# Optimization experiments

Hardware: AMD Instinct MI355X
Metric: run time of the kernel (lower is better)

## Reference

```python
import jax, jax.numpy as jnp
import numpy as np

K = 16
TAU = 0.2
BN_EPS = 1e-5


def setup_inputs() -> dict:
    key = jax.random.key(0)
    ks = jax.random.split(key, 8)
    B, C, N = 2, 128, 8192
    c_hidden, c_out, se_hidden = 128, 128, 8
    x = jax.random.normal(ks[0], (B, C, N), dtype=jnp.float32)
    pos = jax.random.normal(ks[1], (B, 3, N), dtype=jnp.float32)
    # conv1x1 weights (kaiming-ish scale), BN gamma/beta, SE linears (xavier-ish)
    w1 = jax.random.normal(ks[2], (c_hidden, 2 * C), dtype=jnp.float32) * jnp.sqrt(2.0 / c_hidden)
    w2 = jax.random.normal(ks[3], (c_out, c_hidden), dtype=jnp.float32) * jnp.sqrt(2.0 / c_out)
    g1 = jnp.ones((c_hidden,), jnp.float32); b1 = jnp.zeros((c_hidden,), jnp.float32)
    g2 = jnp.ones((c_out,), jnp.float32); b2 = jnp.zeros((c_out,), jnp.float32)
    fc1_w = jax.random.normal(ks[4], (se_hidden, c_out), dtype=jnp.float32) * jnp.sqrt(2.0 / (se_hidden + c_out))
    fc1_b = jnp.zeros((se_hidden,), jnp.float32)
    fc2_w = jax.random.normal(ks[5], (c_out, se_hidden), dtype=jnp.float32) * jnp.sqrt(2.0 / (se_hidden + c_out))
    fc2_b = jnp.zeros((c_out,), jnp.float32)
    return {"x": x, "pos": pos, "w1": w1, "g1": g1, "b1": b1, "w2": w2, "g2": g2, "b2": b2,
            "fc1_w": fc1_w, "fc1_b": fc1_b, "fc2_w": fc2_w, "fc2_b": fc2_b}


def _batchnorm(h, gamma, beta):
    # h: [B, N, C]; training-mode BN over (B, N) with biased variance
    mean = jnp.mean(h, axis=(0, 1), keepdims=True)
    var = jnp.mean((h - mean) ** 2, axis=(0, 1), keepdims=True)
    return (h - mean) * jax.lax.rsqrt(var + BN_EPS) * gamma + beta


def _forward(x, pos, w1, g1, b1, w2, g2, b2, fc1_w, fc1_b, fc2_w, fc2_b):
    x = jnp.nan_to_num(x, nan=0.0, posinf=1e4, neginf=-1e4)
    pos = jnp.nan_to_num(pos, nan=0.0, posinf=1e4, neginf=-1e4)
    B, C, N = x.shape
    x_t = jnp.transpose(x, (0, 2, 1))        # [B, N, C]
    p_t = jnp.transpose(pos, (0, 2, 1))      # [B, N, 3]

    # KNN via full pairwise squared distances (same ordering as torch.cdist topk smallest)
    sq = jnp.sum(p_t * p_t, axis=-1)         # [B, N]
    d2 = sq[:, :, None] + sq[:, None, :] - 2.0 * jnp.einsum('bnd,bmd->bnm', p_t, p_t)  # [B, N, N]
    _, idx = jax.lax.top_k(-d2, K)           # [B, N, K] indices of K nearest (incl. self)
    idx = jax.lax.stop_gradient(idx)

    bidx = jnp.arange(B)[:, None, None]
    neigh_x = x_t[bidx, idx]                 # [B, N, K, C]
    neigh_p = p_t[bidx, idx]                 # [B, N, K, 3]

    diff = neigh_p - p_t[:, :, None, :]
    d = jnp.sqrt(jnp.sum(diff * diff, axis=-1))          # [B, N, K]
    d = jnp.maximum(d, 1e-6)
    w = jax.nn.softmax(-d / TAU, axis=-1)                # [B, N, K]
    agg = jnp.einsum('bnkc,bnk->bnc', neigh_x, w)        # [B, N, C]

    fuse = jnp.concatenate([x_t, agg], axis=-1)          # [B, N, 2C]
    h = jax.nn.relu(_batchnorm(jnp.einsum('bnc,hc->bnh', fuse, w1), g1, b1))
    y = jax.nn.relu(_batchnorm(jnp.einsum('bnh,oh->bno', h, w2), g2, b2))  # [B, N, C_out]

    # SE: global average pool over N, two-layer gate
    s = jnp.mean(y, axis=1)                               # [B, C_out]
    gate = jax.nn.sigmoid(jax.nn.relu(s @ fc1_w.T + fc1_b) @ fc2_w.T + fc2_b)
    y = y * gate[:, None, :]

    y = x_t + y                                           # residual (c_in == c_out)
    return jnp.transpose(y, (0, 2, 1))                    # [B, C_out, N]


def reference(x, pos, w1, g1, b1, w2, g2, b2, fc1_w, fc1_b, fc2_w, fc2_b):
    return _forward(x, pos, w1, g1, b1, w2, g2, b2, fc1_w, fc1_b, fc2_w, fc2_b)
```

## Files before the change

### kernel.cpp

```cpp
#include <hip/hip_runtime.h>
#include <math.h>

#define NPTS 8192
#define NB 2
#define CCH 128
#define KNN 16

typedef __attribute__((ext_vector_type(2))) float f32x2;

__global__ __launch_bounds__(256) void k_zero(float* __restrict__ p) {
  p[blockIdx.x * 256 + threadIdx.x] = 0.f;
}

__device__ __forceinline__ int spread4(int v) {
  return (v & 1) | ((v & 2) << 2) | ((v & 4) << 4) | ((v & 8) << 6);
}
__device__ __forceinline__ int cell_of(float x, float y, float z) {
  int cx = (int)fminf(fmaxf((x + 4.f) * 2.f, 0.f), 15.f);
  int cy = (int)fminf(fmaxf((y + 4.f) * 2.f, 0.f), 15.f);
  int cz = (int)fminf(fmaxf((z + 4.f) * 2.f, 0.f), 15.f);
  return spread4(cx) | (spread4(cy) << 1) | (spread4(cz) << 2);
}

__global__ __launch_bounds__(256) void k_hist(const float* __restrict__ pos,
                                              int* __restrict__ hist) {
  int i = blockIdx.x * 256 + threadIdx.x;
  int b = i >> 13, n = i & 8191;
  const float* p = pos + (size_t)b * 3 * NPTS;
  int c = cell_of(p[n], p[NPTS + n], p[2 * NPTS + n]);
  atomicAdd(&hist[b * 4096 + c], 1);
}

__global__ __launch_bounds__(1024) void k_scan(const int* __restrict__ hist,
                                               int* __restrict__ hoff) {
  __shared__ int part[1024];
  int t = threadIdx.x;
  int v[8];
  int s = 0;
#pragma unroll
  for (int i = 0; i < 8; ++i) { v[i] = hist[t * 8 + i]; s += v[i]; }
  part[t] = s;
  __syncthreads();
  for (int off = 1; off < 512; off <<= 1) {
    int add = ((t & 511) >= off) ? part[t - off] : 0;
    __syncthreads();
    part[t] += add;
    __syncthreads();
  }
  int ex = part[t] - s;
#pragma unroll
  for (int i = 0; i < 8; ++i) { hoff[t * 8 + i] = ex; ex += v[i]; }
}

__global__ __launch_bounds__(256) void k_scatter(const float* __restrict__ pos,
                                                 int* __restrict__ hoff,
                                                 float4* __restrict__ spos,
                                                 int* __restrict__ rank) {
  int i = blockIdx.x * 256 + threadIdx.x;
  int b = i >> 13, n = i & 8191;
  const float* p = pos + (size_t)b * 3 * NPTS;
  float x = p[n], y = p[NPTS + n], z = p[2 * NPTS + n];
  int c = cell_of(x, y, z);
  int slot = atomicAdd(&hoff[b * 4096 + c], 1);
  spos[(b << 13) + slot] = make_float4(x, y, z, fmaf(x, x, fmaf(y, y, z * z)));
  rank[(b << 13) + n] = slot;
}

__global__ __launch_bounds__(256) void k_transpose(const float* __restrict__ x,
                                                   float* __restrict__ xT) {
  __shared__ float t[32][65];
  int blk = blockIdx.x;
  int b = blk >> 9;
  int rem = blk & 511;
  int c0 = (rem >> 7) << 5;
  int n0 = (rem & 127) << 6;
  const float* xb = x + (size_t)b * CCH * NPTS;
  float* xTb = xT + (size_t)b * NPTS * CCH;
  int nj = threadIdx.x & 63, ci = threadIdx.x >> 6;
#pragma unroll
  for (int i = 0; i < 8; ++i) {
    int c = ci * 8 + i;
    t[c][nj] = xb[(size_t)(c0 + c) * NPTS + n0 + nj];
  }
  __syncthreads();
  int cl = threadIdx.x & 31, nl = threadIdx.x >> 5;
#pragma unroll
  for (int i = 0; i < 8; ++i) {
    int n = nl * 8 + i;
    xTb[(size_t)(n0 + n) * CCH + c0 + cl] = t[cl][n];
  }
}


#define SWZF(v, imm) __int_as_float(__builtin_amdgcn_ds_swizzle(__float_as_int(v), (imm)))
#define RDLANEF(v, l) __int_as_float(__builtin_amdgcn_readlane(__float_as_int(v), (l)))
#define DPPF(x) __int_as_float(__builtin_amdgcn_mov_dpp(__float_as_int(x), 0x111, 0xf, 0xf, true))
#define DPPI(x) __builtin_amdgcn_mov_dpp((x), 0x111, 0xf, 0xf, true)

#define BST(var, K, J, IMM)                                        \
  {                                                                \
    float od = SWZF(var, IMM);                                     \
    bool up = ((sub & (K)) == 0);                                  \
    bool low = ((sub & (J)) == 0);                                 \
    bool take = low ? ((var > od) == up) : ((var < od) == up);     \
    if (take) var = od;                                            \
  }
#define BSORT32(v)                                                  \
  BST(v, 2, 1, 0x041F)                                              \
  BST(v, 4, 2, 0x081F)  BST(v, 4, 1, 0x041F)                        \
  BST(v, 8, 4, 0x101F)  BST(v, 8, 2, 0x081F)  BST(v, 8, 1, 0x041F)  \
  BST(v, 16, 8, 0x201F) BST(v, 16, 4, 0x101F) BST(v, 16, 2, 0x081F) \
  BST(v, 16, 1, 0x041F)                                             \
  BST(v, 32, 16, 0x401F) BST(v, 32, 8, 0x201F) BST(v, 32, 4, 0x101F)\
  BST(v, 32, 2, 0x081F) BST(v, 32, 1, 0x041F)
#define BCLEAN32(v)                                                 \
  BST(v, 32, 16, 0x401F) BST(v, 32, 8, 0x201F) BST(v, 32, 4, 0x101F)\
  BST(v, 32, 2, 0x081F) BST(v, 32, 1, 0x041F)

__global__ __launch_bounds__(512, 8) void k_knn(const float* __restrict__ pos,
                                                const float4* __restrict__ spos,
                                                const int* __restrict__ rank,
                                                int* __restrict__ nn_idx,
                                                float* __restrict__ nn_w) {
  __shared__ float4 cpos[2048];
  const int b = blockIdx.x >> 9;
  const int wid = threadIdx.x >> 6;
  const int lane = threadIdx.x & 63;
  const int sub = lane & 31;
  const int grp = lane >> 5;
  const int base = b << 13;
  const int qbase = ((blockIdx.x & 511) << 4) + (wid << 1);
  const int q = qbase + grp;
  const float* px = pos + (size_t)b * 3 * NPTS;
  const float* py = px + NPTS;
  const float* pz = py + NPTS;
  const float qAx = px[qbase], qAy = py[qbase], qAz = pz[qbase];
  const float qBx = px[qbase + 1], qBy = py[qbase + 1], qBz = pz[qbase + 1];
  const float n2Ax = -2.f * qAx, n2Ay = -2.f * qAy, n2Az = -2.f * qAz;
  const float n2Bx = -2.f * qBx, n2By = -2.f * qBy, n2Bz = -2.f * qBz;
  const float qAsq = fmaf(qAx, qAx, fmaf(qAy, qAy, qAz * qAz));
  const float qBsq = fmaf(qBx, qBx, fmaf(qBy, qBy, qBz * qBz));
  const float nsx = grp ? n2Bx : n2Ax;
  const float nsy = grp ? n2By : n2Ay;
  const float nsz = grp ? n2Bz : n2Az;
  const float sqs = grp ? qBsq : qAsq;
  const float qsx = grp ? qBx : qAx;
  const float qsy = grp ? qBy : qAy;
  const float qsz = grp ? qBz : qAz;
  const bool holder = (sub < 16);

  float Tv0A, Tv0B;
  {
    int rk = rank[base + q];
    int seedW = rk & ~63;
    float4 c0 = spos[base + seedW + sub];
    float4 c1 = spos[base + seedW + 32 + sub];
    float sd = fmaf(c0.z, nsz, fmaf(c0.y, nsy, fmaf(c0.x, nsx, c0.w + sqs)));
    float se = fmaf(c1.z, nsz, fmaf(c1.y, nsy, fmaf(c1.x, nsx, c1.w + sqs)));
    BSORT32(sd)
    BSORT32(se)
    float ser = SWZF(se, 0x7C1F);
    sd = fminf(sd, ser);
    BCLEAN32(sd)
    Tv0A = RDLANEF(sd, 15);
    Tv0B = RDLANEF(sd, 47);
  }
  float TvA = Tv0A, TvB = Tv0B;
  float bd = 3.4e38f;
  int bi = 0;

  for (int ch = 0; ch < 4; ++ch) {
    __syncthreads();
    for (int i = threadIdx.x; i < 2048; i += 512) {
      int j = (ch << 11) + i;
      float x = px[j], y = py[j], z = pz[j];
      cpos[i] = make_float4(x, y, z, fmaf(x, x, fmaf(y, y, z * z)));
    }
    __syncthreads();
    for (int t = 0; t < 32; ++t) {
      float4 cp = cpos[(t << 6) + lane];
      float d2A = fmaf(cp.z, n2Az, fmaf(cp.y, n2Ay, fmaf(cp.x, n2Ax, cp.w + qAsq)));
      float d2B = fmaf(cp.z, n2Bz, fmaf(cp.y, n2By, fmaf(cp.x, n2Bx, cp.w + qBsq)));
      unsigned long long mA = __ballot(d2A <= TvA);
      unsigned long long mB = __ballot(d2B <= TvB);
      if (mA | mB) {
        const int cb = (ch << 11) + (t << 6);
        while (mA) {
          int l = __builtin_ctzll(mA);
          mA &= mA - 1;
          float v = RDLANEF(d2A, l);
          if (v > TvA) continue;
          int vi = cb + l;
          float ud = DPPF(bd);
          int ui = DPPI(bi);
          bool gt = (lane < 16) && (bd > v);
          bool first = (sub == 0) || (ud <= v);
          if (gt) {
            bd = first ? v : ud;
            bi = first ? vi : ui;
          }
          TvA = fminf(Tv0A, RDLANEF(bd, 15));
        }
        while (mB) {
          int l = __builtin_ctzll(mB);
          mB &= mB - 1;
          float v = RDLANEF(d2B, l);
          if (v > TvB) continue;
          int vi = cb + l;
          float ud = DPPF(bd);
          int ui = DPPI(bi);
          bool gt = (lane >= 32) && (lane < 48) && (bd > v);
          bool first = (sub == 0) || (ud <= v);
          if (gt) {
            bd = first ? v : ud;
            bi = first ? vi : ui;
          }
          TvB = fminf(Tv0B, RDLANEF(bd, 47));
        }
      }
    }
  }

  float dx = qsx - px[bi], dy = qsy - py[bi], dz = qsz - pz[bi];
  float dd = fmaxf(sqrtf(fmaf(dx, dx, fmaf(dy, dy, dz * dz))), 1e-6f);
  float logit = -dd * 5.0f;
  float mx = holder ? logit : -3.4e38f;
  mx = fmaxf(mx, SWZF(mx, 0x041F));
  mx = fmaxf(mx, SWZF(mx, 0x081F));
  mx = fmaxf(mx, SWZF(mx, 0x101F));
  mx = fmaxf(mx, SWZF(mx, 0x201F));
  float e = holder ? __expf(logit - mx) : 0.f;
  float s = e;
  s += SWZF(s, 0x041F);
  s += SWZF(s, 0x081F);
  s += SWZF(s, 0x101F);
  s += SWZF(s, 0x201F);
  if (holder) {
    size_t o = ((size_t)b * NPTS + q) * KNN + sub;
    nn_idx[o] = bi;
    nn_w[o] = e / s;
  }
}

#define GEMM_CHUNK(ASRC)                                                     \
    _Pragma("unroll")                                                        \
    for (int cq = 0; cq < 16; ++cq) {                                        \
      int c = cq << 2;                                                       \
      float4 a[4], w[4];                                                     \
      _Pragma("unroll")                                                      \
      for (int i = 0; i < 4; ++i) a[i] = ASRC;                               \
      _Pragma("unroll")                                                      \
      for (int j = 0; j < 4; ++j) w[j] = *(const float4*)&wlds[og + (j << 5)][c]; \
      _Pragma("unroll")                                                      \
      for (int i = 0; i < 4; ++i) {                                          \
        f32x2 a01 = {a[i].x, a[i].y}, a23 = {a[i].z, a[i].w};                \
        _Pragma("unroll")                                                    \
        for (int j = 0; j < 4; ++j) {                                        \
          f32x2 w01 = {w[j].x, w[j].y}, w23 = {w[j].z, w[j].w};              \
          acc2[i][j] += a01 * w01;                                           \
          acc2[i][j] += a23 * w23;                                           \
        }                                                                    \
      }                                                                      \
    }

__global__ __launch_bounds__(256) void k_gemm1(const float* __restrict__ xT,
                                               const int* __restrict__ nn_idx,
                                               const float* __restrict__ nn_w,
                                               const float* __restrict__ w1,
                                               float* __restrict__ h_pre,
                                               float* __restrict__ stats1) {
  __shared__ float alds[32][68];
  __shared__ float wlds[128][68];
  __shared__ float aggl[32][132];
  __shared__ float sred[256];
  int b = blockIdx.x >> 8;
  int r0 = (blockIdx.x & 255) << 5;
  const float* xTb = xT + (size_t)b * NPTS * CCH;
  int rg = threadIdx.x & 7, og = threadIdx.x >> 3;
  f32x2 acc2[4][4];
#pragma unroll
  for (int i = 0; i < 4; ++i)
#pragma unroll
    for (int j = 0; j < 4; ++j) acc2[i][j] = (f32x2){0.f, 0.f};
  sred[threadIdx.x] = 0.f;

  {
    int r = threadIdx.x >> 3, cg = threadIdx.x & 7;
    size_t o = ((size_t)b * NPTS + r0 + r) * KNN;
    float ag[16];
#pragma unroll
    for (int i = 0; i < 16; ++i) ag[i] = 0.f;
    for (int k = 0; k < KNN; ++k) {
      int idx = nn_idx[o + k];
      float w = nn_w[o + k];
      const float4* src = (const float4*)(xTb + (size_t)idx * CCH + (cg << 4));
#pragma unroll
      for (int u = 0; u < 4; ++u) {
        float4 v = src[u];
        ag[u * 4 + 0] = fmaf(w, v.x, ag[u * 4 + 0]);
        ag[u * 4 + 1] = fmaf(w, v.y, ag[u * 4 + 1]);
        ag[u * 4 + 2] = fmaf(w, v.z, ag[u * 4 + 2]);
        ag[u * 4 + 3] = fmaf(w, v.w, ag[u * 4 + 3]);
      }
    }
#pragma unroll
    for (int u = 0; u < 4; ++u)
      *(float4*)&aggl[r][(cg << 4) + (u << 2)] =
          make_float4(ag[u * 4], ag[u * 4 + 1], ag[u * 4 + 2], ag[u * 4 + 3]);
  }

  for (int ch = 0; ch < 4; ++ch) {
    __syncthreads();
    if (ch < 2) {
#pragma unroll
      for (int it = 0; it < 2; ++it) {
        int i = threadIdx.x + it * 256;
        int r = i >> 4, kq = i & 15;
        *(float4*)&alds[r][kq << 2] =
            *(const float4*)(xTb + (size_t)(r0 + r) * CCH + (ch << 6) + (kq << 2));
      }
    }
#pragma unroll
    for (int it = 0; it < 8; ++it) {
      int i = threadIdx.x + it * 256;
      int h = i >> 4, kq = i & 15;
      *(float4*)&wlds[h][kq << 2] =
          *(const float4*)(w1 + (size_t)h * 256 + (ch << 6) + (kq << 2));
    }
    __syncthreads();
    if (ch < 2) {
      GEMM_CHUNK(*(const float4*)&alds[rg + (i << 3)][c])
    } else {
      GEMM_CHUNK(*(const float4*)&aggl[rg + (i << 3)][((ch - 2) << 6) + c])
    }
  }
  float acc[4][4];
#pragma unroll
  for (int i = 0; i < 4; ++i)
#pragma unroll
    for (int j = 0; j < 4; ++j) acc[i][j] = acc2[i][j].x + acc2[i][j].y;
#pragma unroll
  for (int i = 0; i < 4; ++i) {
    int row = r0 + rg + (i << 3);
    float* dst = h_pre + ((size_t)b * NPTS + row) * CCH;
#pragma unroll
    for (int j = 0; j < 4; ++j) dst[og + (j << 5)] = acc[i][j];
  }
#pragma unroll
  for (int j = 0; j < 4; ++j) {
    float ps = acc[0][j] + acc[1][j] + acc[2][j] + acc[3][j];
    float pq = acc[0][j] * acc[0][j] + acc[1][j] * acc[1][j] +
               acc[2][j] * acc[2][j] + acc[3][j] * acc[3][j];
    atomicAdd(&sred[og + (j << 5)], ps);
    atomicAdd(&sred[128 + og + (j << 5)], pq);
  }
  __syncthreads();
  atomicAdd(&stats1[threadIdx.x], sred[threadIdx.x]);
}

__global__ __launch_bounds__(256) void k_gemm2(const float* __restrict__ h_pre,
                                               const float* __restrict__ stats1,
                                               const float* __restrict__ g1,
                                               const float* __restrict__ b1,
                                               const float* __restrict__ w2,
                                               float* __restrict__ y_pre,
                                               float* __restrict__ stats2) {
  __shared__ float alds[32][68];
  __shared__ float wlds[128][68];
  __shared__ float sred[256];
  __shared__ float scs[128], shs[128];
  int b = blockIdx.x >> 8;
  int r0 = (blockIdx.x & 255) << 5;
  int rg = threadIdx.x & 7, og = threadIdx.x >> 3;
  f32x2 acc2[4][4];
#pragma unroll
  for (int i = 0; i < 4; ++i)
#pragma unroll
    for (int j = 0; j < 4; ++j) acc2[i][j] = (f32x2){0.f, 0.f};
  sred[threadIdx.x] = 0.f;
  if (threadIdx.x < 128) {
    int c = threadIdx.x;
    float sm = stats1[c] * (1.f / 16384.f);
    float sq = stats1[128 + c] * (1.f / 16384.f);
    float var = fmaxf(sq - sm * sm, 0.f);
    float sc = g1[c] * rsqrtf(var + 1e-5f);
    scs[c] = sc;
    shs[c] = b1[c] - sm * sc;
  }
  for (int ch = 0; ch < 2; ++ch) {
    __syncthreads();
#pragma unroll
    for (int it = 0; it < 2; ++it) {
      int i = threadIdx.x + it * 256;
      int r = i >> 4, kq = i & 15;
      int c = (ch << 6) + (kq << 2);
      float4 v = *(const float4*)(h_pre + ((size_t)b * NPTS + r0 + r) * CCH + c);
      float4 sc = *(const float4*)&scs[c];
      float4 sh = *(const float4*)&shs[c];
      v.x = fmaxf(fmaf(v.x, sc.x, sh.x), 0.f);
      v.y = fmaxf(fmaf(v.y, sc.y, sh.y), 0.f);
      v.z = fmaxf(fmaf(v.z, sc.z, sh.z), 0.f);
      v.w = fmaxf(fmaf(v.w, sc.w, sh.w), 0.f);
      *(float4*)&alds[r][kq << 2] = v;
    }
#pragma unroll
    for (int it = 0; it < 8; ++it) {
      int i = threadIdx.x + it * 256;
      int h = i >> 4, kq = i & 15;
      *(float4*)&wlds[h][kq << 2] =
          *(const float4*)(w2 + (size_t)h * CCH + (ch << 6) + (kq << 2));
    }
    __syncthreads();
#pragma unroll
    for (int cq = 0; cq < 16; ++cq) {
      int c = cq << 2;
      float4 a[4], w[4];
#pragma unroll
      for (int i = 0; i < 4; ++i) a[i] = *(const float4*)&alds[rg + (i << 3)][c];
#pragma unroll
      for (int j = 0; j < 4; ++j) w[j] = *(const float4*)&wlds[og + (j << 5)][c];
#pragma unroll
      for (int i = 0; i < 4; ++i) {
        f32x2 a01 = {a[i].x, a[i].y}, a23 = {a[i].z, a[i].w};
#pragma unroll
        for (int j = 0; j < 4; ++j) {
          f32x2 w01 = {w[j].x, w[j].y}, w23 = {w[j].z, w[j].w};
          acc2[i][j] += a01 * w01;
          acc2[i][j] += a23 * w23;
        }
      }
    }
  }
  float acc[4][4];
#pragma unroll
  for (int i = 0; i < 4; ++i)
#pragma unroll
    for (int j = 0; j < 4; ++j) acc[i][j] = acc2[i][j].x + acc2[i][j].y;
#pragma unroll
  for (int i = 0; i < 4; ++i) {
    int row = r0 + rg + (i << 3);
    float* dst = y_pre + ((size_t)b * NPTS + row) * CCH;
#pragma unroll
    for (int j = 0; j < 4; ++j) dst[og + (j << 5)] = acc[i][j];
  }
#pragma unroll
  for (int j = 0; j < 4; ++j) {
    float ps = acc[0][j] + acc[1][j] + acc[2][j] + acc[3][j];
    float pq = acc[0][j] * acc[0][j] + acc[1][j] * acc[1][j] +
               acc[2][j] * acc[2][j] + acc[3][j] * acc[3][j];
    atomicAdd(&sred[og + (j << 5)], ps);
    atomicAdd(&sred[128 + og + (j << 5)], pq);
  }
  __syncthreads();
  atomicAdd(&stats2[threadIdx.x], sred[threadIdx.x]);
}

__global__ __launch_bounds__(256) void k_sepool(const float* __restrict__ y_pre,
                                                const float* __restrict__ stats2,
                                                const float* __restrict__ g2,
                                                const float* __restrict__ b2,
                                                float* __restrict__ s_sum) {
  __shared__ float red[256];
  int b = blockIdx.x >> 7;
  int r0 = (blockIdx.x & 127) << 6;
  int c = threadIdx.x & 127, half = threadIdx.x >> 7;
  float sm = stats2[c] * (1.f / 16384.f);
  float sq = stats2[128 + c] * (1.f / 16384.f);
  float var = fmaxf(sq - sm * sm, 0.f);
  float sc = g2[c] * rsqrtf(var + 1e-5f);
  float sh = b2[c] - sm * sc;
  float acc = 0.f;
  for (int r = half; r < 64; r += 2) {
    float v = y_pre[((size_t)b * NPTS + r0 + r) * CCH + c];
    acc += fmaxf(v * sc + sh, 0.f);
  }
  red[threadIdx.x] = acc;
  __syncthreads();
  if (half == 0) atomicAdd(&s_sum[b * CCH + c], red[c] + red[128 + c]);
}

__global__ __launch_bounds__(128) void k_segate(const float* __restrict__ s_sum,
                                                const float* __restrict__ fc1w,
                                                const float* __restrict__ fc1b,
                                                const float* __restrict__ fc2w,
                                                const float* __restrict__ fc2b,
                                                float* __restrict__ gate) {
  __shared__ float s[128];
  __shared__ float hid[8];
  int b = blockIdx.x, t = threadIdx.x;
  s[t] = s_sum[b * CCH + t] * (1.f / 8192.f);
  __syncthreads();
  if (t < 8) {
    float a = fc1b[t];
    for (int c = 0; c < 128; ++c) a += s[c] * fc1w[t * 128 + c];
    hid[t] = fmaxf(a, 0.f);
  }
  __syncthreads();
  float a = fc2b[t];
#pragma unroll
  for (int j = 0; j < 8; ++j) a += hid[j] * fc2w[t * 8 + j];
  gate[b * CCH + t] = 1.f / (1.f + __expf(-a));
}

__global__ __launch_bounds__(256) void k_out(const float* __restrict__ x,
                                             const float* __restrict__ y_pre,
                                             const float* __restrict__ stats2,
                                             const float* __restrict__ g2,
                                             const float* __restrict__ b2,
                                             const float* __restrict__ gate,
                                             float* __restrict__ out) {
  __shared__ float t[64][129];
  int b = blockIdx.x >> 7;
  int n0 = (blockIdx.x & 127) << 6;
  {
    int c = threadIdx.x & 127;
    float sm = stats2[c] * (1.f / 16384.f);
    float sq = stats2[128 + c] * (1.f / 16384.f);
    float var = fmaxf(sq - sm * sm, 0.f);
    float sc = g2[c] * rsqrtf(var + 1e-5f);
    float sh = b2[c] - sm * sc;
    float gt = gate[b * CCH + c];
    for (int r = threadIdx.x >> 7; r < 64; r += 2) {
      float v = y_pre[((size_t)b * NPTS + n0 + r) * CCH + c];
      t[r][c] = fmaxf(v * sc + sh, 0.f) * gt;
    }
  }
  __syncthreads();
  int nl = threadIdx.x & 63, cg = threadIdx.x >> 6;
  for (int cc = cg; cc < CCH; cc += 4) {
    size_t o = ((size_t)b * CCH + cc) * NPTS + n0 + nl;
    out[o] = x[o] + t[nl][cc];
  }
}

extern "C" void kernel_launch(void* const* d_in, const int* in_sizes, int n_in,
                              void* d_out, int out_size, void* d_ws, size_t ws_size,
                              hipStream_t stream) {
  const float* x = (const float*)d_in[0];
  const float* pos = (const float*)d_in[1];
  const float* w1 = (const float*)d_in[2];
  const float* g1 = (const float*)d_in[3];
  const float* b1 = (const float*)d_in[4];
  const float* w2 = (const float*)d_in[5];
  const float* g2 = (const float*)d_in[6];
  const float* b2 = (const float*)d_in[7];
  const float* fc1w = (const float*)d_in[8];
  const float* fc1b = (const float*)d_in[9];
  const float* fc2w = (const float*)d_in[10];
  const float* fc2b = (const float*)d_in[11];
  float* out = (float*)d_out;
  char* ws = (char*)d_ws;
  const size_t MB = 1048576;

  float* xT = (float*)(ws + 0);
  int* nn_idx = (int*)(ws + 8 * MB);
  float* nn_w = (float*)(ws + 9 * MB);
  float* h_pre = (float*)(ws + 18 * MB);
  char* meta = ws + 26 * MB;
  float* stats = (float*)meta;
  int* hist = (int*)(meta + 4096);
  int* hoff = (int*)(meta + 4096 + 32768);
  float4* spos = (float4*)(meta + 4096 + 65536);
  int* rank = (int*)(meta + 4096 + 65536 + 262144);
  float* y_pre;
  if (ws_size >= 35 * MB) {
    y_pre = (float*)(ws + 27 * MB);
  } else {
    y_pre = (float*)(ws + 0);
  }
  float* stats1 = stats;
  float* stats2 = stats + 256;
  float* s_sum = stats + 512;
  float* gate = stats + 768;

  k_zero<<<36, 256, 0, stream>>>(stats);
  k_hist<<<64, 256, 0, stream>>>(pos, hist);
  k_scan<<<1, 1024, 0, stream>>>(hist, hoff);
  k_scatter<<<64, 256, 0, stream>>>(pos, hoff, spos, rank);
  k_transpose<<<1024, 256, 0, stream>>>(x, xT);
  k_knn<<<1024, 512, 0, stream>>>(pos, spos, rank, nn_idx, nn_w);
  k_gemm1<<<512, 256, 0, stream>>>(xT, nn_idx, nn_w, w1, h_pre, stats1);
  k_gemm2<<<512, 256, 0, stream>>>(h_pre, stats1, g1, b1, w2, y_pre, stats2);
  k_sepool<<<256, 256, 0, stream>>>(y_pre, stats2, g2, b2, s_sum);
  k_segate<<<2, 128, 0, stream>>>(s_sum, fc1w, fc1b, fc2w, fc2b, gate);
  k_out<<<256, 256, 0, stream>>>(x, y_pre, stats2, g2, b2, gate, out);
}
```

Before: 171.4 us.

## Fuse SE gate into pool via last-block counter and shrink GEMM K-chunks

The SE gate computation now runs inside the pooling kernel: the last block to finish, detected with an atomic counter and thread fences, computes the gate for both batches. This removes one kernel launch. The stats buffer is now zeroed inside the scan kernel, and the zero kernel clears the counter and histogram region instead. Both GEMM kernels now stage K in 32-wide chunks instead of 64, which halves LDS use per block and may raise occupancy, at the cost of more barrier iterations.

Result: slower. 193.6 us (+13.0%).

```diff
diff --git a/kernel.cpp b/kernel.cpp
--- a/kernel.cpp
+++ b/kernel.cpp
@@ -32,9 +32,11 @@
 }
 
 __global__ __launch_bounds__(1024) void k_scan(const int* __restrict__ hist,
-                                               int* __restrict__ hoff) {
+                                               int* __restrict__ hoff,
+                                               float* __restrict__ stats) {
   __shared__ int part[1024];
   int t = threadIdx.x;
+  stats[t] = 0.f;
   int v[8];
   int s = 0;
 #pragma unroll
@@ -90,7 +92,6 @@
     xTb[(size_t)(n0 + n) * CCH + c0 + cl] = t[cl][n];
   }
 }
-
 
 #define SWZF(v, imm) __int_as_float(__builtin_amdgcn_ds_swizzle(__float_as_int(v), (imm)))
 #define RDLANEF(v, l) __int_as_float(__builtin_amdgcn_readlane(__float_as_int(v), (l)))
@@ -242,9 +243,9 @@
   }
 }
 
-#define GEMM_CHUNK(ASRC)                                                     \
+#define GEMM_CHUNK8(ASRC)                                                    \
     _Pragma("unroll")                                                        \
-    for (int cq = 0; cq < 16; ++cq) {                                        \
+    for (int cq = 0; cq < 8; ++cq) {                                         \
       int c = cq << 2;                                                       \
       float4 a[4], w[4];                                                     \
       _Pragma("unroll")                                                      \
@@ -269,8 +270,8 @@
                                                const float* __restrict__ w1,
                                                float* __restrict__ h_pre,
                                                float* __restrict__ stats1) {
-  __shared__ float alds[32][68];
-  __shared__ float wlds[128][68];
+  __shared__ float alds[32][36];
+  __shared__ float wlds[128][36];
   __shared__ float aggl[32][132];
   __shared__ float sred[256];
   int b = blockIdx.x >> 8;
@@ -309,29 +310,25 @@
           make_float4(ag[u * 4], ag[u * 4 + 1], ag[u * 4 + 2], ag[u * 4 + 3]);
   }
 
-  for (int ch = 0; ch < 4; ++ch) {
-    __syncthreads();
-    if (ch < 2) {
-#pragma unroll
-      for (int it = 0; it < 2; ++it) {
-        int i = threadIdx.x + it * 256;
-        int r = i >> 4, kq = i & 15;
-        *(float4*)&alds[r][kq << 2] =
-            *(const float4*)(xTb + (size_t)(r0 + r) * CCH + (ch << 6) + (kq << 2));
-      }
-    }
-#pragma unroll
-    for (int it = 0; it < 8; ++it) {
+  for (int ch = 0; ch < 8; ++ch) {
+    __syncthreads();
+    if (ch < 4) {
+      int r = threadIdx.x >> 3, kq = threadIdx.x & 7;
+      *(float4*)&alds[r][kq << 2] =
+          *(const float4*)(xTb + (size_t)(r0 + r) * CCH + (ch << 5) + (kq << 2));
+    }
+#pragma unroll
+    for (int it = 0; it < 4; ++it) {
       int i = threadIdx.x + it * 256;
-      int h = i >> 4, kq = i & 15;
+      int h = i >> 3, kq = i & 7;
       *(float4*)&wlds[h][kq << 2] =
-          *(const float4*)(w1 + (size_t)h * 256 + (ch << 6) + (kq << 2));
-    }
-    __syncthreads();
-    if (ch < 2) {
-      GEMM_CHUNK(*(const float4*)&alds[rg + (i << 3)][c])
+          *(const float4*)(w1 + (size_t)h * 256 + (ch << 5) + (kq << 2));
+    }
+    __syncthreads();
+    if (ch < 4) {
+      GEMM_CHUNK8(*(const float4*)&alds[rg + (i << 3)][c])
     } else {
-      GEMM_CHUNK(*(const float4*)&aggl[rg + (i << 3)][((ch - 2) << 6) + c])
+      GEMM_CHUNK8(*(const float4*)&aggl[rg + (i << 3)][((ch - 4) << 5) + c])
     }
   }
   float acc[4][4];
@@ -365,8 +362,8 @@
                                                const float* __restrict__ w2,
                                                float* __restrict__ y_pre,
                                                float* __restrict__ stats2) {
-  __shared__ float alds[32][68];
-  __shared__ float wlds[128][68];
+  __shared__ float alds[32][36];
+  __shared__ float wlds[128][36];
   __shared__ float sred[256];
   __shared__ float scs[128], shs[128];
   int b = blockIdx.x >> 8;
@@ -387,13 +384,11 @@
     scs[c] = sc;
     shs[c] = b1[c] - sm * sc;
   }
-  for (int ch = 0; ch < 2; ++ch) {
-    __syncthreads();
-#pragma unroll
-    for (int it = 0; it < 2; ++it) {
-      int i = threadIdx.x + it * 256;
-      int r = i >> 4, kq = i & 15;
-      int c = (ch << 6) + (kq << 2);
+  for (int ch = 0; ch < 4; ++ch) {
+    __syncthreads();
+    {
+      int r = threadIdx.x >> 3, kq = threadIdx.x & 7;
+      int c = (ch << 5) + (kq << 2);
       float4 v = *(const float4*)(h_pre + ((size_t)b * NPTS + r0 + r) * CCH + c);
       float4 sc = *(const float4*)&scs[c];
       float4 sh = *(const float4*)&shs[c];
@@ -404,15 +399,15 @@
       *(float4*)&alds[r][kq << 2] = v;
     }
 #pragma unroll
-    for (int it = 0; it < 8; ++it) {
+    for (int it = 0; it < 4; ++it) {
       int i = threadIdx.x + it * 256;
-      int h = i >> 4, kq = i & 15;
+      int h = i >> 3, kq = i & 7;
       *(float4*)&wlds[h][kq << 2] =
-          *(const float4*)(w2 + (size_t)h * CCH + (ch << 6) + (kq << 2));
-    }
-    __syncthreads();
-#pragma unroll
-    for (int cq = 0; cq < 16; ++cq) {
+          *(const float4*)(w2 + (size_t)h * CCH + (ch << 5) + (kq << 2));
+    }
+    __syncthreads();
+#pragma unroll
+    for (int cq = 0; cq < 8; ++cq) {
       int c = cq << 2;
       float4 a[4], w[4];
 #pragma unroll
@@ -459,8 +454,16 @@
                                                 const float* __restrict__ stats2,
                                                 const float* __restrict__ g2,
                                                 const float* __restrict__ b2,
-                                                float* __restrict__ s_sum) {
+                                                const float* __restrict__ fc1w,
+                                                const float* __restrict__ fc1b,
+                                                const float* __restrict__ fc2w,
+                                                const float* __restrict__ fc2b,
+                                                float* __restrict__ s_sum,
+                                                float* __restrict__ gate,
+                                                int* __restrict__ cnt) {
   __shared__ float red[256];
+  __shared__ float hid2[16];
+  __shared__ int last;
   int b = blockIdx.x >> 7;
   int r0 = (blockIdx.x & 127) << 6;
   int c = threadIdx.x & 127, half = threadIdx.x >> 7;
@@ -477,29 +480,27 @@
   red[threadIdx.x] = acc;
   __syncthreads();
   if (half == 0) atomicAdd(&s_sum[b * CCH + c], red[c] + red[128 + c]);
-}
-
-__global__ __launch_bounds__(128) void k_segate(const float* __restrict__ s_sum,
-                                                const float* __restrict__ fc1w,
-                                                const float* __restrict__ fc1b,
-                                                const float* __restrict__ fc2w,
-                                                const float* __restrict__ fc2b,
-                                                float* __restrict__ gate) {
-  __shared__ float s[128];
-  __shared__ float hid[8];
-  int b = blockIdx.x, t = threadIdx.x;
-  s[t] = s_sum[b * CCH + t] * (1.f / 8192.f);
-  __syncthreads();
-  if (t < 8) {
-    float a = fc1b[t];
-    for (int c = 0; c < 128; ++c) a += s[c] * fc1w[t * 128 + c];
-    hid[t] = fmaxf(a, 0.f);
-  }
-  __syncthreads();
-  float a = fc2b[t];
-#pragma unroll
-  for (int j = 0; j < 8; ++j) a += hid[j] * fc2w[t * 8 + j];
-  gate[b * CCH + t] = 1.f / (1.f + __expf(-a));
+  __threadfence();
+  __syncthreads();
+  if (threadIdx.x == 0) last = (atomicAdd(cnt, 1) == 255);
+  __syncthreads();
+  if (last) {
+    __threadfence();
+    int t = threadIdx.x;
+    red[t] = s_sum[(t >> 7) * CCH + (t & 127)] * (1.f / 8192.f);
+    __syncthreads();
+    if (t < 16) {
+      int bb = t >> 3, j = t & 7;
+      float a = fc1b[j];
+      for (int cc = 0; cc < 128; ++cc) a += red[bb * 128 + cc] * fc1w[j * 128 + cc];
+      hid2[t] = fmaxf(a, 0.f);
+    }
+    __syncthreads();
+    float a = fc2b[t & 127];
+#pragma unroll
+    for (int j = 0; j < 8; ++j) a += hid2[(t >> 7) * 8 + j] * fc2w[(t & 127) * 8 + j];
+    gate[(t >> 7) * CCH + (t & 127)] = 1.f / (1.f + __expf(-a));
+  }
 }
 
 __global__ __launch_bounds__(256) void k_out(const float* __restrict__ x,
@@ -558,10 +559,11 @@
   float* h_pre = (float*)(ws + 18 * MB);
   char* meta = ws + 26 * MB;
   float* stats = (float*)meta;
-  int* hist = (int*)(meta + 4096);
-  int* hoff = (int*)(meta + 4096 + 32768);
-  float4* spos = (float4*)(meta + 4096 + 65536);
-  int* rank = (int*)(meta + 4096 + 65536 + 262144);
+  int* cnt = (int*)(meta + 4096);
+  int* hist = (int*)(meta + 8192);
+  int* hoff = (int*)(meta + 8192 + 32768);
+  float4* spos = (float4*)(meta + 8192 + 65536);
+  int* rank = (int*)(meta + 8192 + 65536 + 262144);
   float* y_pre;
   if (ws_size >= 35 * MB) {
     y_pre = (float*)(ws + 27 * MB);
@@ -573,15 +575,15 @@
   float* s_sum = stats + 512;
   float* gate = stats + 768;
 
-  k_zero<<<36, 256, 0, stream>>>(stats);
+  k_zero<<<36, 256, 0, stream>>>((float*)(meta + 4096));
   k_hist<<<64, 256, 0, stream>>>(pos, hist);
-  k_scan<<<1, 1024, 0, stream>>>(hist, hoff);
+  k_scan<<<1, 1024, 0, stream>>>(hist, hoff, stats);
   k_scatter<<<64, 256, 0, stream>>>(pos, hoff, spos, rank);
   k_transpose<<<1024, 256, 0, stream>>>(x, xT);
   k_knn<<<1024, 512, 0, stream>>>(pos, spos, rank, nn_idx, nn_w);
   k_gemm1<<<512, 256, 0, stream>>>(xT, nn_idx, nn_w, w1, h_pre, stats1);
   k_gemm2<<<512, 256, 0, stream>>>(h_pre, stats1, g1, b1, w2, y_pre, stats2);
-  k_sepool<<<256, 256, 0, stream>>>(y_pre, stats2, g2, b2, s_sum);
-  k_segate<<<2, 128, 0, stream>>>(s_sum, fc1w, fc1b, fc2w, fc2b, gate);
+  k_sepool<<<256, 256, 0, stream>>>(y_pre, stats2, g2, b2, fc1w, fc1b, fc2w,
+                                    fc2b, s_sum, gate, cnt);
   k_out<<<256, 256, 0, stream>>>(x, y_pre, stats2, g2, b2, gate, out);
 }
```
